# Kernel optimization log

Measured on AMD Instinct MI355X. Metric: run time of the kernel, lower is better.

## Reference

```python
import jax, jax.numpy as jnp
import numpy as np

B, N_TOK, C, M, H = 4, 2048, 256, 64, 8


def setup_inputs() -> dict:
    key = jax.random.key(0)
    ks = jax.random.split(key, 10)
    s = 0.02
    return {
        "x1": jax.random.normal(ks[0], (B, N_TOK, C), dtype=jnp.float32),
        "x2": jax.random.normal(ks[1], (B, N_TOK, C), dtype=jnp.float32),
        "cor": jax.random.normal(ks[2], (B, N_TOK, 3), dtype=jnp.float32),
        "Wq": jax.random.normal(ks[3], (C, C), dtype=jnp.float32) * s,
        "Wkv": jax.random.normal(ks[4], (C, 2 * C), dtype=jnp.float32) * s,
        "Wcor": jax.random.normal(ks[5], (3, M), dtype=jnp.float32) * s,
        "Wproj": jax.random.normal(ks[6], (C, C), dtype=jnp.float32) * s,
        "bproj": jnp.zeros((C,), dtype=jnp.float32),
        "Wm": jax.random.normal(ks[7], (M, M), dtype=jnp.float32) * s,
        "bm": jnp.zeros((M,), dtype=jnp.float32),
        "N": N_TOK,
    }


def reference(x1, x2, cor, Wq, Wkv, Wcor, Wproj, bproj, Wm, bm, N):
    B_, n, C_ = x1.shape
    Dh = C_ // H                      # head dim = 32
    scale = Dh ** (-0.5)
    # projections (no bias on q/kv/cor_embed, qkv_bias=False)
    q = (x1 @ Wq).reshape(B_, n, H, Dh).transpose(0, 2, 1, 3)          # [B,H,N,Dh]
    kv = (x2 @ Wkv).reshape(B_, n, 2, H, Dh)
    k = kv[:, :, 0].transpose(0, 2, 1, 3)                              # [B,H,N,Dh]
    v = kv[:, :, 1].transpose(0, 2, 1, 3)                              # [B,H,N,Dh]
    cor_embed_ = cor @ Wcor                                            # [B,N,M]
    Mh = cor_embed_.shape[-1] // H
    cor_embed = cor_embed_.reshape(B_, n, H, Mh).transpose(0, 2, 1, 3) # [B,H,N,Mh]
    # attention (mask=None path); weights reused for two value matmuls
    attn = jax.nn.softmax(jnp.einsum('bhnd,bhmd->bhnm', q, k) * scale, axis=-1)
    x = jnp.einsum('bhnm,bhmd->bnhd', attn, v).reshape(B_, n, C_)
    c_reverse = jnp.einsum('bhnm,bhmd->bnhd', attn, cor_embed).reshape(B_, n, -1)
    motion = (c_reverse - cor_embed_) @ Wm + bm
    x = x @ Wproj + bproj
    return (x, motion)
```

## Files before the change

kernel.cpp:

```cpp
#include <hip/hip_runtime.h>

#define B_ 4
#define NTOK 2048
#define CCH 256
#define HH 8
#define DH 32
#define MM 64
#define DV 48
#define ROWS (B_*NTOK)

typedef __bf16 bf16_t;
typedef bf16_t bf16x8 __attribute__((ext_vector_type(8)));
typedef float f32x4 __attribute__((ext_vector_type(4)));
typedef unsigned int u32x4 __attribute__((ext_vector_type(4)));
typedef unsigned short u16;

#define QSCALE (0.17677669529663687f * 1.44269504088896340f)

__device__ __forceinline__ u16 f2bf(float x) {
    unsigned u = __builtin_bit_cast(unsigned, x);
    return (u16)((u + 0x7FFFu + ((u >> 16) & 1u)) >> 16);
}
__device__ __forceinline__ unsigned cvt_pk(float lo, float hi) {
    unsigned r;
    asm("v_cvt_pk_bf16_f32 %0, %1, %2" : "=v"(r) : "v"(lo), "v"(hi));
    return r;
}
__device__ __forceinline__ f32x4 mfma16(bf16x8 a, bf16x8 b, f32x4 c) {
    return __builtin_amdgcn_mfma_f32_16x16x32_bf16(a, b, c, 0, 0, 0);
}
#if __has_builtin(__builtin_amdgcn_exp2f)
#define EXP2(x) __builtin_amdgcn_exp2f(x)
#else
#define EXP2(x) exp2f(x)
#endif

__device__ __forceinline__ bf16x8 exp_transpose(f32x4 s0, f32x4 s1) {
    unsigned W0 = cvt_pk(EXP2(s0[0]), EXP2(s0[1]));
    unsigned W1 = cvt_pk(EXP2(s0[2]), EXP2(s0[3]));
    unsigned W2 = cvt_pk(EXP2(s1[0]), EXP2(s1[1]));
    unsigned W3 = cvt_pk(EXP2(s1[2]), EXP2(s1[3]));
    asm("v_permlane32_swap_b32 %0, %1" : "+v"(W0), "+v"(W2));
    asm("v_permlane32_swap_b32 %0, %1" : "+v"(W1), "+v"(W3));
    asm("v_permlane16_swap_b32 %0, %1" : "+v"(W0), "+v"(W2));
    asm("v_permlane16_swap_b32 %0, %1" : "+v"(W1), "+v"(W3));
    u32x4 pw; pw[0] = W0; pw[1] = W1; pw[2] = W2; pw[3] = W3;
    return __builtin_bit_cast(bf16x8, pw);
}

__global__ __launch_bounds__(256) void prep_k(
    const float* __restrict__ x1, const float* __restrict__ x2,
    const float* __restrict__ Wq, const float* __restrict__ Wkv,
    const float* __restrict__ Wproj, const float* __restrict__ cor,
    const float* __restrict__ Wcor, const float* __restrict__ Wm,
    u16* __restrict__ x1b, u16* __restrict__ x2b,
    u16* __restrict__ Wqt, u16* __restrict__ Wkvt, u16* __restrict__ Wprojt,
    u16* __restrict__ Vt, float* __restrict__ G) {
    int bx = blockIdx.x, tid = threadIdx.x;
    if (bx < 2048) {
        const float* X = (bx < 1024) ? x1 : x2;
        u16* Xb = (bx < 1024) ? x1b : x2b;
        size_t i = (size_t)(bx & 1023) * 256 + tid;
        f32x4 a0 = *(const f32x4*)(X + i * 8);
        f32x4 a1 = *(const f32x4*)(X + i * 8 + 4);
        u32x4 w;
        w[0] = cvt_pk(a0[0], a0[1]);
        w[1] = cvt_pk(a0[2], a0[3]);
        w[2] = cvt_pk(a1[0], a1[1]);
        w[3] = cvt_pk(a1[2], a1[3]);
        *(u32x4*)(Xb + i * 8) = w;
    } else if (bx < 3072) {
        int r = bx - 2048;
        const float* W; u16* Wt; int N, base;
        if (r < 256)      { W = Wq;    Wt = Wqt;    N = 256; base = r; }
        else if (r < 768) { W = Wkv;   Wt = Wkvt;   N = 512; base = r - 256; }
        else              { W = Wproj; Wt = Wprojt; N = 256; base = r - 768; }
        int i = base * 256 + tid;
        int k = i / N, n = i - k * N;
        Wt[(size_t)n * 256 + k] = f2bf(W[i]);
    } else if (bx < 3104) {
        int bh = bx - 3072;
        int b2 = bh >> 3;
        for (int n = tid; n < NTOK; n += 256) {
            const float* cp = cor + ((size_t)b2 * NTOK + n) * 3;
            u16* vp = Vt + ((size_t)bh * DV + 32) * NTOK + n;
            vp[0]        = f2bf(cp[0]);
            vp[NTOK]     = f2bf(cp[1]);
            vp[2 * NTOK] = f2bf(cp[2]);
            vp[3 * NTOK] = (u16)0x3F80;
        }
    } else {
        int idx = (bx - 3104) * 256 + tid;
        int m = idx & 63, hj = idx >> 6;
        int hh = hj / 3, j = hj - 3 * hh;
        float acc = 0.f;
#pragma unroll
        for (int t = 0; t < 8; t++)
            acc += Wcor[j * 64 + hh * 8 + t] * Wm[(hh * 8 + t) * 64 + m];
        G[idx] = acc;
    }
}

__global__ __launch_bounds__(256, 6) void qkv_k(
    const u16* __restrict__ x1b, const u16* __restrict__ x2b,
    const u16* __restrict__ Wqt, const u16* __restrict__ Wkvt,
    u16* __restrict__ Qh, u16* __restrict__ Kh, u16* __restrict__ Vt) {
    __shared__ u16 panel[64][72];
    int tid = threadIdx.x;
    int lane = tid & 63, wave = tid >> 6;
    int g = lane >> 4, q = lane & 15;
    int m0 = blockIdx.x * 64 + wave * 16;
    bool isq = blockIdx.y < 4;
    bool isv = blockIdx.y >= 8;
    const u16* Ab = isq ? x1b : x2b;
    const u16* Bt = isq ? Wqt : Wkvt;
    int c0 = (isq ? blockIdx.y : blockIdx.y - 4) * 64;
    f32x4 acc[4] = {};
#pragma unroll
    for (int k0 = 0; k0 < CCH; k0 += 32) {
        bf16x8 af = *(const bf16x8*)(Ab + (size_t)(m0 + q) * CCH + k0 + g * 8);
#pragma unroll
        for (int t = 0; t < 4; t++) {
            bf16x8 bfr = *(const bf16x8*)(Bt + (size_t)(c0 + t * 16 + q) * CCH + k0 + g * 8);
            acc[t] = mfma16(af, bfr, acc[t]);
        }
    }
#pragma unroll
    for (int t = 0; t < 4; t++) {
#pragma unroll
        for (int r = 0; r < 4; r++) {
            int rl = wave * 16 + 4 * g + r;
            int cl = t * 16 + q;
            float v = acc[t][r];
            if (isq) v *= QSCALE;
            u16 val = f2bf(v);
            if (isv) panel[cl][rl] = val;
            else     panel[rl][cl] = val;
        }
    }
    __syncthreads();
    int a = tid >> 2, ch = tid & 3;
    union { u16 u[16]; u32x4 v[2]; } buf;
#pragma unroll
    for (int j = 0; j < 16; j++) buf.u[j] = panel[a][ch * 16 + j];
    u16* dst;
    if (!isv) {
        int row = blockIdx.x * 64 + a;
        int b = row >> 11, n = row & 2047;
        int c = c0 + ch * 16;
        dst = (isq ? Qh : Kh) + ((size_t)(b * HH + (c >> 5)) * NTOK + n) * DH + (c & 31);
    } else {
        int cc = (blockIdx.y - 8) * 64 + a;
        int n0 = blockIdx.x * 64 + ch * 16;
        int b = n0 >> 11, n = n0 & 2047;
        dst = Vt + ((size_t)(b * HH + (cc >> 5)) * DV + (cc & 31)) * NTOK + n;
    }
    *(u32x4*)(dst) = buf.v[0];
    *(u32x4*)(dst + 8) = buf.v[1];
}

__global__ __launch_bounds__(256, 2) void attn_k(
    const u16* __restrict__ Qh, const u16* __restrict__ Kh, const u16* __restrict__ Vt,
    u16* __restrict__ xpre, float* __restrict__ pc) {
    __shared__ __align__(16) float cb[4][3][64][12];
    int bh = blockIdx.x;
    int b = bh >> 3, h = bh & 7;
    int ks = threadIdx.x >> 6;
    int lane = threadIdx.x & 63;
    int g = lane >> 4, q = lane & 15;
    int qbase = blockIdx.y * 64;

    const u16* Qp = Qh + ((size_t)bh * NTOK + qbase + q) * DH + g * 8;
    bf16x8 qf0 = *(const bf16x8*)Qp;
    bf16x8 qf1 = *(const bf16x8*)(Qp + 16 * DH);
    bf16x8 qf2 = *(const bf16x8*)(Qp + 32 * DH);
    bf16x8 qf3 = *(const bf16x8*)(Qp + 48 * DH);

    const u16* kp = Kh + (size_t)bh * NTOK * DH + (size_t)(ks * 512 + q) * DH + g * 8;
    const u16* Vb = Vt + (size_t)bh * DV * NTOK + (size_t)q * NTOK + ks * 512 + g * 8;

    f32x4 acc00 = {}, acc01 = {}, acc02 = {}, acc10 = {}, acc11 = {}, acc12 = {};
    f32x4 acc20 = {}, acc21 = {}, acc22 = {}, acc30 = {}, acc31 = {}, acc32 = {};
    const f32x4 zacc = {0.f, 0.f, 0.f, 0.f};
    int voff = 0;

#pragma unroll 1
    for (int t = 0; t < 16; t++) {
        bf16x8 ka = *(const bf16x8*)(kp);
        bf16x8 kb = *(const bf16x8*)(kp + 16 * DH);
        kp += 32 * DH;
        bf16x8 va = *(const bf16x8*)(Vb + voff);
        bf16x8 vb = *(const bf16x8*)(Vb + 16 * NTOK + voff);
        bf16x8 vc = *(const bf16x8*)(Vb + 32 * NTOK + voff);
        voff += 32;
        {
            f32x4 s0 = mfma16(ka, qf0, zacc);
            f32x4 s1 = mfma16(kb, qf0, zacc);
            bf16x8 pf = exp_transpose(s0, s1);
            acc00 = mfma16(pf, va, acc00);
            acc01 = mfma16(pf, vb, acc01);
            acc02 = mfma16(pf, vc, acc02);
        }
        {
            f32x4 s0 = mfma16(ka, qf1, zacc);
            f32x4 s1 = mfma16(kb, qf1, zacc);
            bf16x8 pf = exp_transpose(s0, s1);
            acc10 = mfma16(pf, va, acc10);
            acc11 = mfma16(pf, vb, acc11);
            acc12 = mfma16(pf, vc, acc12);
        }
        {
            f32x4 s0 = mfma16(ka, qf2, zacc);
            f32x4 s1 = mfma16(kb, qf2, zacc);
            bf16x8 pf = exp_transpose(s0, s1);
            acc20 = mfma16(pf, va, acc20);
            acc21 = mfma16(pf, vb, acc21);
            acc22 = mfma16(pf, vc, acc22);
        }
        {
            f32x4 s0 = mfma16(ka, qf3, zacc);
            f32x4 s1 = mfma16(kb, qf3, zacc);
            bf16x8 pf = exp_transpose(s0, s1);
            acc30 = mfma16(pf, va, acc30);
            acc31 = mfma16(pf, vb, acc31);
            acc32 = mfma16(pf, vc, acc32);
        }
    }

#define ST3(dst, x, y, z) { *(f32x4*)(dst) = x; *(f32x4*)((dst) + 4) = y; *(f32x4*)((dst) + 8) = z; }
    {
        float* s0 = &cb[ks][0][lane][0];
        float* s1 = &cb[ks][1][lane][0];
        float* s2 = &cb[ks][2][lane][0];
        switch (ks) {
            case 0: ST3(s0, acc10, acc11, acc12) ST3(s1, acc20, acc21, acc22) ST3(s2, acc30, acc31, acc32) break;
            case 1: ST3(s0, acc20, acc21, acc22) ST3(s1, acc30, acc31, acc32) ST3(s2, acc00, acc01, acc02) break;
            case 2: ST3(s0, acc30, acc31, acc32) ST3(s1, acc00, acc01, acc02) ST3(s2, acc10, acc11, acc12) break;
            default: ST3(s0, acc00, acc01, acc02) ST3(s1, acc10, acc11, acc12) ST3(s2, acc20, acc21, acc22) break;
        }
    }
    __syncthreads();
    f32x4 A0, A1, A2;
    switch (ks) {
        case 0:  A0 = acc00; A1 = acc01; A2 = acc02; break;
        case 1:  A0 = acc10; A1 = acc11; A2 = acc12; break;
        case 2:  A0 = acc20; A1 = acc21; A2 = acc22; break;
        default: A0 = acc30; A1 = acc31; A2 = acc32; break;
    }
#pragma unroll
    for (int d = 1; d < 4; d++) {
        int s = (ks + d) & 3;
        int j = (ks - s - 1) & 3;
        const float* r = &cb[s][j][lane][0];
        A0 += *(const f32x4*)(r);
        A1 += *(const f32x4*)(r + 4);
        A2 += *(const f32x4*)(r + 8);
    }

    float inv[4];
#pragma unroll
    for (int r = 0; r < 4; r++) inv[r] = 1.0f / __shfl(A2[r], (lane & 48) | 3, 64);
#pragma unroll
    for (int r = 0; r < 4; r++) {
        size_t nrow = (size_t)b * NTOK + qbase + ks * 16 + 4 * g + r;
        u16* xp = xpre + nrow * CCH + h * DH;
        xp[q] = f2bf(A0[r] * inv[r]);
        xp[16 + q] = f2bf(A1[r] * inv[r]);
        if (q < 3) pc[nrow * 24 + h * 3 + q] = A2[r] * inv[r];
    }
}

__global__ __launch_bounds__(256) void out_k(
    const u16* __restrict__ xpre, const u16* __restrict__ Wprojt,
    const float* __restrict__ bias, const float* __restrict__ pc,
    const float* __restrict__ cor, const float* __restrict__ G,
    const float* __restrict__ bm, float* __restrict__ o_x,
    float* __restrict__ o_m) {
    __shared__ float Gs[24][64];
    __shared__ float u[4][24];
    int tid = threadIdx.x;
    if (blockIdx.x < 512) {
        int bx = blockIdx.x;
        int lane = tid & 63, wave = tid >> 6;
        int g = lane >> 4, q = lane & 15;
        int m0 = (bx >> 2) * 64 + wave * 16;
        int c0 = (bx & 3) * 64;
        f32x4 acc[4] = {};
#pragma unroll
        for (int k0 = 0; k0 < CCH; k0 += 32) {
            bf16x8 af = *(const bf16x8*)(xpre + (size_t)(m0 + q) * CCH + k0 + g * 8);
#pragma unroll
            for (int t = 0; t < 4; t++) {
                bf16x8 bfr = *(const bf16x8*)(Wprojt + (size_t)(c0 + t * 16 + q) * CCH + k0 + g * 8);
                acc[t] = mfma16(af, bfr, acc[t]);
            }
        }
#pragma unroll
        for (int t = 0; t < 4; t++) {
#pragma unroll
            for (int r = 0; r < 4; r++) {
                int row = m0 + 4 * g + r;
                int c = c0 + t * 16 + q;
                o_x[(size_t)row * CCH + c] = acc[t][r] + bias[c];
            }
        }
    } else {
        for (int i = tid; i < 1536; i += 256) Gs[i >> 6][i & 63] = G[i];
        size_t tok0 = (size_t)(blockIdx.x - 512) * 4;
        if (tid < 96) {
            int tl = tid / 24, e = tid - tl * 24;
            int j = e % 3;
            size_t token = tok0 + tl;
            u[tl][e] = pc[token * 24 + e] - cor[token * 3 + j];
        }
        __syncthreads();
        int tl = tid >> 6, m = tid & 63;
        float v = bm[m];
#pragma unroll
        for (int e = 0; e < 24; e++) v += u[tl][e] * Gs[e][m];
        o_m[(tok0 + tl) * 64 + m] = v;
    }
}

extern "C" void kernel_launch(void* const* d_in, const int* in_sizes, int n_in,
                              void* d_out, int out_size, void* d_ws, size_t ws_size,
                              hipStream_t stream) {
    const float* x1    = (const float*)d_in[0];
    const float* x2    = (const float*)d_in[1];
    const float* cor   = (const float*)d_in[2];
    const float* Wq    = (const float*)d_in[3];
    const float* Wkv   = (const float*)d_in[4];
    const float* Wcor  = (const float*)d_in[5];
    const float* Wproj = (const float*)d_in[6];
    const float* bproj = (const float*)d_in[7];
    const float* Wm    = (const float*)d_in[8];
    const float* bm    = (const float*)d_in[9];
    float* out_x = (float*)d_out;
    float* out_motion = out_x + (size_t)ROWS * CCH;

    u16* Wqt    = (u16*)d_ws;
    u16* Wkvt   = Wqt + 65536;
    u16* Wprojt = Wkvt + 131072;
    u16* x1b    = Wprojt + 65536;
    u16* x2b    = x1b + (size_t)2097152;
    u16* Qh     = x2b + (size_t)2097152;
    u16* Kh     = Qh + (size_t)2097152;
    u16* Vt     = Kh + (size_t)2097152;
    u16* xpre   = Vt + (size_t)3145728;
    float* pcb  = (float*)(xpre + (size_t)2097152);
    float* G    = pcb + (size_t)ROWS * 24;

    prep_k<<<3110, 256, 0, stream>>>(x1, x2, Wq, Wkv, Wproj, cor, Wcor, Wm,
                                     x1b, x2b, Wqt, Wkvt, Wprojt, Vt, G);
    qkv_k<<<dim3(128, 12), 256, 0, stream>>>(x1b, x2b, Wqt, Wkvt, Qh, Kh, Vt);
    attn_k<<<dim3(32, 32), 256, 0, stream>>>(Qh, Kh, Vt, xpre, pcb);
    out_k<<<2560, 256, 0, stream>>>(xpre, Wprojt, bproj, pcb, cor, G, bm,
                                    out_x, out_motion);
}
```

Measured before the change: 93.71 us.

## Halve attention query tile to 32 rows with two-way key split

The attention kernel now processes 32 query rows per block with 2 waves, each covering half the keys (1024), instead of 64 rows with 4 waves each covering a quarter. Launches 2048 smaller blocks and cuts the shared-memory cross-wave reduction to a single pairwise add. Each loaded K/V fragment is reused across only 2 query subtiles instead of 4, so K/V traffic per query doubles. In exchange there are fewer accumulator registers, more blocks and a cheaper reduction.

```diff
diff --git a/kernel.cpp b/kernel.cpp
--- a/kernel.cpp
+++ b/kernel.cpp
@@ -159,33 +159,31 @@
     *(u32x4*)(dst + 8) = buf.v[1];
 }
 
-__global__ __launch_bounds__(256, 2) void attn_k(
+__global__ __launch_bounds__(128, 2) void attn_k(
     const u16* __restrict__ Qh, const u16* __restrict__ Kh, const u16* __restrict__ Vt,
     u16* __restrict__ xpre, float* __restrict__ pc) {
-    __shared__ __align__(16) float cb[4][3][64][12];
+    __shared__ __align__(16) float cb[2][64][12];
     int bh = blockIdx.x;
     int b = bh >> 3, h = bh & 7;
     int ks = threadIdx.x >> 6;
     int lane = threadIdx.x & 63;
     int g = lane >> 4, q = lane & 15;
-    int qbase = blockIdx.y * 64;
+    int qbase = blockIdx.y * 32;
 
     const u16* Qp = Qh + ((size_t)bh * NTOK + qbase + q) * DH + g * 8;
     bf16x8 qf0 = *(const bf16x8*)Qp;
     bf16x8 qf1 = *(const bf16x8*)(Qp + 16 * DH);
-    bf16x8 qf2 = *(const bf16x8*)(Qp + 32 * DH);
-    bf16x8 qf3 = *(const bf16x8*)(Qp + 48 * DH);
-
-    const u16* kp = Kh + (size_t)bh * NTOK * DH + (size_t)(ks * 512 + q) * DH + g * 8;
-    const u16* Vb = Vt + (size_t)bh * DV * NTOK + (size_t)q * NTOK + ks * 512 + g * 8;
-
-    f32x4 acc00 = {}, acc01 = {}, acc02 = {}, acc10 = {}, acc11 = {}, acc12 = {};
-    f32x4 acc20 = {}, acc21 = {}, acc22 = {}, acc30 = {}, acc31 = {}, acc32 = {};
+
+    const u16* kp = Kh + (size_t)bh * NTOK * DH + (size_t)(ks * 1024 + q) * DH + g * 8;
+    const u16* Vb = Vt + (size_t)bh * DV * NTOK + (size_t)q * NTOK + ks * 1024 + g * 8;
+
+    f32x4 acc00 = {}, acc01 = {}, acc02 = {};
+    f32x4 acc10 = {}, acc11 = {}, acc12 = {};
     const f32x4 zacc = {0.f, 0.f, 0.f, 0.f};
     int voff = 0;
 
 #pragma unroll 1
-    for (int t = 0; t < 16; t++) {
+    for (int t = 0; t < 32; t++) {
         bf16x8 ka = *(const bf16x8*)(kp);
         bf16x8 kb = *(const bf16x8*)(kp + 16 * DH);
         kp += 32 * DH;
@@ -209,52 +207,21 @@
             acc11 = mfma16(pf, vb, acc11);
             acc12 = mfma16(pf, vc, acc12);
         }
-        {
-            f32x4 s0 = mfma16(ka, qf2, zacc);
-            f32x4 s1 = mfma16(kb, qf2, zacc);
-            bf16x8 pf = exp_transpose(s0, s1);
-            acc20 = mfma16(pf, va, acc20);
-            acc21 = mfma16(pf, vb, acc21);
-            acc22 = mfma16(pf, vc, acc22);
-        }
-        {
-            f32x4 s0 = mfma16(ka, qf3, zacc);
-            f32x4 s1 = mfma16(kb, qf3, zacc);
-            bf16x8 pf = exp_transpose(s0, s1);
-            acc30 = mfma16(pf, va, acc30);
-            acc31 = mfma16(pf, vb, acc31);
-            acc32 = mfma16(pf, vc, acc32);
-        }
     }
 
 #define ST3(dst, x, y, z) { *(f32x4*)(dst) = x; *(f32x4*)((dst) + 4) = y; *(f32x4*)((dst) + 8) = z; }
     {
-        float* s0 = &cb[ks][0][lane][0];
-        float* s1 = &cb[ks][1][lane][0];
-        float* s2 = &cb[ks][2][lane][0];
-        switch (ks) {
-            case 0: ST3(s0, acc10, acc11, acc12) ST3(s1, acc20, acc21, acc22) ST3(s2, acc30, acc31, acc32) break;
-            case 1: ST3(s0, acc20, acc21, acc22) ST3(s1, acc30, acc31, acc32) ST3(s2, acc00, acc01, acc02) break;
-            case 2: ST3(s0, acc30, acc31, acc32) ST3(s1, acc00, acc01, acc02) ST3(s2, acc10, acc11, acc12) break;
-            default: ST3(s0, acc00, acc01, acc02) ST3(s1, acc10, acc11, acc12) ST3(s2, acc20, acc21, acc22) break;
-        }
+        float* s = &cb[ks][lane][0];
+        if (ks == 0) { ST3(s, acc10, acc11, acc12) }
+        else         { ST3(s, acc00, acc01, acc02) }
     }
     __syncthreads();
     f32x4 A0, A1, A2;
-    switch (ks) {
-        case 0:  A0 = acc00; A1 = acc01; A2 = acc02; break;
-        case 1:  A0 = acc10; A1 = acc11; A2 = acc12; break;
-        case 2:  A0 = acc20; A1 = acc21; A2 = acc22; break;
-        default: A0 = acc30; A1 = acc31; A2 = acc32; break;
-    }
-#pragma unroll
-    for (int d = 1; d < 4; d++) {
-        int s = (ks + d) & 3;
-        int j = (ks - s - 1) & 3;
-        const float* r = &cb[s][j][lane][0];
-        A0 += *(const f32x4*)(r);
-        A1 += *(const f32x4*)(r + 4);
-        A2 += *(const f32x4*)(r + 8);
+    {
+        const float* r = &cb[1 ^ ks][lane][0];
+        A0 = (ks ? acc10 : acc00) + *(const f32x4*)(r);
+        A1 = (ks ? acc11 : acc01) + *(const f32x4*)(r + 4);
+        A2 = (ks ? acc12 : acc02) + *(const f32x4*)(r + 8);
     }
 
     float inv[4];
@@ -353,7 +320,7 @@
     prep_k<<<3110, 256, 0, stream>>>(x1, x2, Wq, Wkv, Wproj, cor, Wcor, Wm,
                                      x1b, x2b, Wqt, Wkvt, Wprojt, Vt, G);
     qkv_k<<<dim3(128, 12), 256, 0, stream>>>(x1b, x2b, Wqt, Wkvt, Qh, Kh, Vt);
-    attn_k<<<dim3(32, 32), 256, 0, stream>>>(Qh, Kh, Vt, xpre, pcb);
+    attn_k<<<dim3(32, 64), 128, 0, stream>>>(Qh, Kh, Vt, xpre, pcb);
     out_k<<<2560, 256, 0, stream>>>(xpre, Wprojt, bproj, pcb, cor, G, bm,
                                     out_x, out_motion);
 }
```

After: 120.6 us. 28.7% more time.
